# Performance work log

Measured on AMD Instinct MI355X. Metric: run time of the kernel, lower is better.

The kernel has to match this reference:

```python
import jax, jax.numpy as jnp
import numpy as np

B, S, D, H = 8, 1025, 768, 12
HD = D // H  # 64

def setup_inputs() -> dict:
    key = jax.random.key(0)
    ks = jax.random.split(key, 5)
    scale = 0.02
    return {
        "hidden_states": jax.random.normal(ks[0], (B, S, D), jnp.float32),
        "rel_bias": jax.random.normal(ks[1], (1, H, S, S), jnp.float32),
        "Wq": jax.random.normal(ks[2], (D, D), jnp.float32) * scale,
        "bq": jnp.zeros((D,), jnp.float32),
        "Wk": jax.random.normal(ks[3], (D, D), jnp.float32) * scale,
        "bk": jnp.zeros((D,), jnp.float32),
        "Wv": jax.random.normal(ks[4], (D, D), jnp.float32) * scale,
        "bv": jnp.zeros((D,), jnp.float32),
    }

def reference(hidden_states, rel_bias, Wq, bq, Wk, bk, Wv, bv):
    b, s, d = hidden_states.shape
    def split_heads(t):  # [B,S,D] -> [B,H,S,hd]
        return t.reshape(b, s, H, HD).transpose(0, 2, 1, 3)
    q = split_heads(hidden_states @ Wq + bq)
    k = split_heads(hidden_states @ Wk + bk)
    v = split_heads(hidden_states @ Wv + bv)
    inv_sqrt_hd = 1.0 / jnp.sqrt(jnp.asarray(HD, q.dtype))
    scores = jnp.einsum("bhqd,bhkd->bhqk", q, k) * inv_sqrt_hd
    scores = scores + rel_bias  # broadcast [1,H,S,S]
    probs = jax.nn.softmax(scores, axis=-1)
    ctx = jnp.einsum("bhqk,bhkd->bhqd", probs, v)
    out = ctx.transpose(0, 2, 1, 3).reshape(b, s, d)
    return out
```

## Files before the change

kernel.cpp:

```cpp
#include <hip/hip_runtime.h>

using f32x4  = __attribute__((ext_vector_type(4))) float;
using bf16x8 = __attribute__((ext_vector_type(8))) short;

#define SEQ 1025
#define NH  12

__device__ __forceinline__ unsigned short f2bf(float f) {
  unsigned u = __float_as_uint(f);
  u += 0x7FFFu + ((u >> 16) & 1u);
  return (unsigned short)(u >> 16);
}

__device__ __forceinline__ unsigned short f2bf_p(float f) {
  return (unsigned short)((__float_as_uint(f) + 0x8000u) >> 16);
}

__device__ __forceinline__ void async16(const void* g, void* s) {
  __builtin_amdgcn_global_load_lds(
      (const __attribute__((address_space(1))) void*)g,
      (__attribute__((address_space(3))) void*)s, 16, 0, 0);
}

__global__ __launch_bounds__(256) void conv_x(const float* __restrict__ X,
                                              ushort* __restrict__ Xb) {
  int t = blockIdx.x * 256 + threadIdx.x;
  if (t >= 8320 * 96) return;
  int row = t / 96;
  size_t e = (size_t)t * 8;
  union { uint4 q; ushort us[8]; } o;
  if (row < 8200) {
    float4 f0 = *(const float4*)(X + e);
    float4 f1 = *(const float4*)(X + e + 4);
    o.us[0] = f2bf(f0.x); o.us[1] = f2bf(f0.y); o.us[2] = f2bf(f0.z); o.us[3] = f2bf(f0.w);
    o.us[4] = f2bf(f1.x); o.us[5] = f2bf(f1.y); o.us[6] = f2bf(f1.z); o.us[7] = f2bf(f1.w);
  } else {
    o.q = make_uint4(0, 0, 0, 0);
  }
  *(uint4*)(Xb + e) = o.q;
}

__global__ __launch_bounds__(256) void pack_w(const float* __restrict__ Wq,
                                              const float* __restrict__ Wk,
                                              const float* __restrict__ Wv,
                                              ushort* __restrict__ Wt) {
  __shared__ float tile[32][33];
  const int nt = blockIdx.x;
  const int kt = blockIdx.y;
  const int sel = nt / 24;
  const int o0 = (nt - sel * 24) * 32;
  const int k0 = kt * 32;
  const float* W = sel == 0 ? Wq : sel == 1 ? Wk : Wv;
  const int t = threadIdx.x;
  const int x = t & 31, y = t >> 5;
  for (int p = 0; p < 4; ++p)
    tile[y + p * 8][x] = W[(size_t)(k0 + y + p * 8) * 768 + o0 + x];
  __syncthreads();
  for (int p = 0; p < 4; ++p) {
    const int nl = y + p * 8;
    Wt[(size_t)(nt * 32 + nl) * 768 + k0 + x] = f2bf(tile[x][nl]);
  }
}

__global__ __launch_bounds__(256) void pack_bias(const float* __restrict__ bq,
                                                 const float* __restrict__ bk,
                                                 const float* __restrict__ bv,
                                                 float* __restrict__ bc) {
  int t = blockIdx.x * 256 + threadIdx.x;
  if (t < 768) bc[t] = bq[t];
  else if (t < 1536) bc[t] = bk[t - 768];
  else if (t < 2304) bc[t] = bv[t - 1536];
}

__global__ __launch_bounds__(256, 2) void repack_bias_frag(
    const float* __restrict__ rel, float* __restrict__ bf) {
  __shared__ float lds[16][1092];
  const int h = blockIdx.x / 72;
  const int w = blockIdx.x - h * 72;
  const int t = threadIdx.x;
  const float* src = rel + (size_t)h * SEQ * SEQ;
  for (int r = 0; r < 16; ++r) {
    int q = w * 16 + r; if (q > 1024) q = 1024;
    const float* row = src + (size_t)q * SEQ;
    for (int c = t; c < 1088; c += 256)
      lds[r][c] = (c <= 1024) ? row[c] * 1.44269504f : -3.0e30f;
  }
  __syncthreads();
  float* dst = bf + ((size_t)h * 17 * 72 + w) * 1024;
  for (int kt = 0; kt < 17; ++kt) {
    float* d = dst + (size_t)kt * (72 * 1024);
    for (int j = t; j < 1024; j += 256) {
      int lane = j >> 4, e = j & 15;
      int ct = e >> 2, r2 = e & 3;
      int row = ((lane >> 4) << 2) + r2;
      int col = kt * 64 + ct * 16 + (lane & 15);
      d[j] = lds[row][col];
    }
  }
}

__global__ __launch_bounds__(256) void gemm_qkv(const ushort* __restrict__ A,
                                                const ushort* __restrict__ Bt,
                                                const float* __restrict__ bias,
                                                ushort* __restrict__ Qo,
                                                ushort* __restrict__ Ko,
                                                ushort* __restrict__ Vo) {
  __shared__ ushort a_sm[128 * 32];
  __shared__ ushort b_sm[128 * 32];
  const int t = threadIdx.x;
  const int lane = t & 63, wave = t >> 6;
  const int quad = lane >> 4, l16 = lane & 15;
  const int wrow = wave >> 1, wcol = wave & 1;
  const int m0 = blockIdx.x * 128, n0 = blockIdx.y * 128;

  f32x4 acc[4][4] = {};

  const ushort* a_g = A + (size_t)m0 * 768;
  const ushort* b_g = Bt + (size_t)n0 * 768;

  for (int k0 = 0; k0 < 768; k0 += 32) {
    __syncthreads();
    for (int r = 0; r < 2; ++r) {
      int c = r * 256 + t;
      int row = c >> 2;
      int colb = (c & 3) * 16;
      async16((const char*)(a_g + (size_t)row * 768 + k0) + colb, (char*)a_sm + c * 16);
      async16((const char*)(b_g + (size_t)row * 768 + k0) + colb, (char*)b_sm + c * 16);
    }
    __syncthreads();
    bf16x8 af[4], bfr[4];
    for (int i = 0; i < 4; ++i) {
      af[i]  = *(const bf16x8*)(a_sm + (wrow * 64 + i * 16 + l16) * 32 + quad * 8);
      bfr[i] = *(const bf16x8*)(b_sm + (wcol * 64 + i * 16 + l16) * 32 + quad * 8);
    }
    for (int i = 0; i < 4; ++i)
      for (int j = 0; j < 4; ++j)
        acc[i][j] = __builtin_amdgcn_mfma_f32_16x16x32_bf16(af[i], bfr[j], acc[i][j], 0, 0, 0);
  }

  for (int j = 0; j < 4; ++j) {
    const int gn = n0 + wcol * 64 + j * 16 + l16;
    const int sel = gn / 768;
    const int o = gn - sel * 768;
    const int hh = o >> 6, hd = o & 63;
    const float bv = bias[gn];
    ushort* dst = sel == 0 ? Qo : sel == 1 ? Ko : Vo;
    for (int i = 0; i < 4; ++i) {
      const int gmb = m0 + wrow * 64 + i * 16 + quad * 4;
      for (int r = 0; r < 4; ++r) {
        const int gm = gmb + r;
        if (gm < 8200) {
          const int bb = gm / 1025;
          const int ss = gm - bb * 1025;
          dst[(((size_t)(bb * NH + hh) * SEQ + ss) << 6) + hd] = f2bf(acc[i][j][r] + bv);
        }
      }
    }
  }
}

__global__ __launch_bounds__(256, 4) void attn(const ushort* __restrict__ Qb,
                                               const ushort* __restrict__ Kb,
                                               const ushort* __restrict__ Vb,
                                               const float* __restrict__ biasF,
                                               float* __restrict__ out) {
  __shared__ char smem[36864];
  ushort* p_sm = (ushort*)smem;
  ushort* k_sm = (ushort*)(smem + 18432);
  ushort* v_sm = (ushort*)(smem + 27648);

  const int t = threadIdx.x;
  const int lane = t & 63, wave = t >> 6;
  const int quad = lane >> 4, l16 = lane & 15;

  const int id = blockIdx.x;
  const int x = id & 7, s = id >> 3;
  const int Gg = s / 9, qt = s - Gg * 9;
  const int G = Gg * 8 + x;
  const int b = G / 12, h = G - b * 12;
  const int q0 = qt * 128;

  const size_t bh = (size_t)(b * NH + h) * SEQ * 64;
  const ushort* Qp = Qb + bh;
  const ushort* Kp = Kb + bh;
  const ushort* Vp = Vb + bh;

  uint4 kpre0, kpre1, vpre0, vpre1;
  const int vkp2 = t & 31, vhb = (t >> 5) * 8;

  auto issue_kv = [&](int kb) {
    {
      int c = t, row = c >> 3, cb = (c & 7) * 8;
      int rk = kb + row; if (rk > 1024) rk = 1024;
      kpre0 = *(const uint4*)(Kp + (size_t)rk * 64 + cb);
    }
    {
      int c = t + 256, row = c >> 3, cb = (c & 7) * 8;
      int rk = kb + row; if (rk > 1024) rk = 1024;
      kpre1 = *(const uint4*)(Kp + (size_t)rk * 64 + cb);
    }
    {
      int r0 = kb + vkp2 * 2;
      int r0c = r0 > 1024 ? 1024 : r0;
      int r1c = r0 + 1 > 1024 ? 1024 : r0 + 1;
      vpre0 = *(const uint4*)(Vp + (size_t)r0c * 64 + vhb);
      vpre1 = *(const uint4*)(Vp + (size_t)r1c * 64 + vhb);
    }
  };

  issue_kv(0);

  ushort* pw = p_sm + wave * (32 * 72);
  const int qbase = q0 + wave * 32;
  for (int i = 0; i < 4; ++i) {
    int c = lane + 64 * i;
    int row = c >> 3, cb = (c & 7) * 8;
    int rq = qbase + row; if (rq > 1024) rq = 1024;
    *(uint4*)(pw + row * 72 + cb) = *(const uint4*)(Qp + (size_t)rq * 64 + cb);
  }
  bf16x8 qf[2][2];
  for (int rt = 0; rt < 2; ++rt)
    for (int ks = 0; ks < 2; ++ks)
      qf[rt][ks] = *(const bf16x8*)(pw + (rt * 16 + l16) * 72 + ks * 32 + quad * 8);

  float lst[8] = {0, 0, 0, 0, 0, 0, 0, 0};
  f32x4 oacc[2][4] = {};
  const float c_scale = 0.18033688f;
  const float* bf_base = biasF +
      ((size_t)h * 17 * 72 + (qt * 8 + wave * 2)) * 1024 + (lane << 4);

  for (int kt = 0; kt < 17; ++kt) {
    __syncthreads();
    {
      int c = t;
      *(uint4*)(k_sm + (c >> 3) * 72 + (c & 7) * 8) = kpre0;
      c = t + 256;
      *(uint4*)(k_sm + (c >> 3) * 72 + (c & 7) * 8) = kpre1;
    }
    {
      union { uint4 q; ushort us[8]; } e0, e1;
      e0.q = vpre0; e1.q = vpre1;
      for (int e = 0; e < 8; ++e)
        *(unsigned*)(v_sm + (vhb + e) * 72 + vkp2 * 2) =
            (unsigned)e0.us[e] | ((unsigned)e1.us[e] << 16);
    }
    __syncthreads();

    const float* bfp = bf_base + (size_t)kt * (72 * 1024);
    f32x4 br[2][4];
    for (int rt = 0; rt < 2; ++rt)
      for (int ct = 0; ct < 4; ++ct)
        br[rt][ct] = *(const f32x4*)(bfp + rt * 1024 + ct * 4);

    if (kt < 16) issue_kv(kt * 64 + 64);

    f32x4 sc[2][4] = {};
    for (int ct = 0; ct < 4; ++ct)
      for (int ks = 0; ks < 2; ++ks) {
        bf16x8 kf = *(const bf16x8*)(k_sm + (ct * 16 + l16) * 72 + ks * 32 + quad * 8);
        sc[0][ct] = __builtin_amdgcn_mfma_f32_16x16x32_bf16(qf[0][ks], kf, sc[0][ct], 0, 0, 0);
        sc[1][ct] = __builtin_amdgcn_mfma_f32_16x16x32_bf16(qf[1][ks], kf, sc[1][ct], 0, 0, 0);
      }

    for (int rt = 0; rt < 2; ++rt)
      for (int ct = 0; ct < 4; ++ct)
        for (int r2 = 0; r2 < 4; ++r2) {
          float p = __builtin_amdgcn_exp2f(
              fmaf(sc[rt][ct][r2], c_scale, br[rt][ct][r2]));
          lst[rt * 4 + r2] += p;
          pw[(rt * 16 + quad * 4 + r2) * 72 + ct * 16 + l16] = f2bf_p(p);
        }

    for (int ks = 0; ks < 2; ++ks) {
      bf16x8 pf0 = *(const bf16x8*)(pw + l16 * 72 + ks * 32 + quad * 8);
      bf16x8 pf1 = *(const bf16x8*)(pw + (16 + l16) * 72 + ks * 32 + quad * 8);
      for (int c4 = 0; c4 < 4; ++c4) {
        bf16x8 vf = *(const bf16x8*)(v_sm + (c4 * 16 + l16) * 72 + ks * 32 + quad * 8);
        oacc[0][c4] = __builtin_amdgcn_mfma_f32_16x16x32_bf16(pf0, vf, oacc[0][c4], 0, 0, 0);
        oacc[1][c4] = __builtin_amdgcn_mfma_f32_16x16x32_bf16(pf1, vf, oacc[1][c4], 0, 0, 0);
      }
    }
  }

  for (int si = 0; si < 8; ++si) {
    float s2 = lst[si];
    s2 += __shfl_xor(s2, 1);
    s2 += __shfl_xor(s2, 2);
    s2 += __shfl_xor(s2, 4);
    s2 += __shfl_xor(s2, 8);
    lst[si] = s2;
  }
  for (int rt = 0; rt < 2; ++rt)
    for (int r2 = 0; r2 < 4; ++r2) {
      int sr = qbase + rt * 16 + quad * 4 + r2;
      if (sr < SEQ) {
        float inv = 1.0f / lst[rt * 4 + r2];
        float* op = out + ((size_t)b * SEQ + sr) * 768 + h * 64;
        for (int c4 = 0; c4 < 4; ++c4)
          op[c4 * 16 + l16] = oacc[rt][c4][r2] * inv;
      }
    }
}

extern "C" void kernel_launch(void* const* d_in, const int* in_sizes, int n_in,
                              void* d_out, int out_size, void* d_ws, size_t ws_size,
                              hipStream_t stream) {
  const float* X  = (const float*)d_in[0];
  const float* rb = (const float*)d_in[1];
  const float* Wq = (const float*)d_in[2];
  const float* bq = (const float*)d_in[3];
  const float* Wk = (const float*)d_in[4];
  const float* bk = (const float*)d_in[5];
  const float* Wv = (const float*)d_in[6];
  const float* bv = (const float*)d_in[7];
  float* out = (float*)d_out;
  char* ws = (char*)d_ws;

  ushort* Qb    = (ushort*)ws;
  ushort* Kb    = (ushort*)(ws + 12595200);
  ushort* Vb    = (ushort*)(ws + 25190400);
  ushort* Xb    = (ushort*)(ws + 37785600);
  ushort* Wt    = (ushort*)(ws + 50565120);
  float*  biasc = (float*)(ws + 54104064);
  float*  biasF = (float*)(ws + 37785600);

  conv_x<<<3120, 256, 0, stream>>>(X, Xb);
  pack_w<<<dim3(72, 24), 256, 0, stream>>>(Wq, Wk, Wv, Wt);
  pack_bias<<<9, 256, 0, stream>>>(bq, bk, bv, biasc);
  gemm_qkv<<<dim3(65, 18), 256, 0, stream>>>(Xb, Wt, biasc, Qb, Kb, Vb);
  repack_bias_frag<<<NH * 72, 256, 0, stream>>>(rb, biasF);
  attn<<<864, 256, 0, stream>>>(Qb, Kb, Vb, biasF, out);
}
```

Measured before the change: 369.6 us.

## Stage QKV epilogue through LDS, split bias repack, fuse bias pack

The QKV GEMM epilogue now stages bf16 results in shared memory and writes 16-byte vectorized rows per head, replacing scattered 2-byte stores. The relative-bias repack kernel is split into two column halves with a smaller LDS footprint, allowing more blocks per CU, and it writes f32x4 vectors. The bias-concatenation kernel is folded into pack_w to remove one launch. The cost is extra LDS and barriers in the GEMM epilogue.

Result: faster. 317.8 us (-14.0%).

```diff
diff --git a/kernel.cpp b/kernel.cpp
--- a/kernel.cpp
+++ b/kernel.cpp
@@ -43,7 +43,17 @@
 __global__ __launch_bounds__(256) void pack_w(const float* __restrict__ Wq,
                                               const float* __restrict__ Wk,
                                               const float* __restrict__ Wv,
-                                              ushort* __restrict__ Wt) {
+                                              ushort* __restrict__ Wt,
+                                              const float* __restrict__ bq,
+                                              const float* __restrict__ bk,
+                                              const float* __restrict__ bv,
+                                              float* __restrict__ bc) {
+  if (blockIdx.y == 0 && blockIdx.x < 9) {
+    int t2 = blockIdx.x * 256 + threadIdx.x;
+    if (t2 < 768) bc[t2] = bq[t2];
+    else if (t2 < 1536) bc[t2] = bk[t2 - 768];
+    else if (t2 < 2304) bc[t2] = bv[t2 - 1536];
+  }
   __shared__ float tile[32][33];
   const int nt = blockIdx.x;
   const int kt = blockIdx.y;
@@ -62,40 +72,38 @@
   }
 }
 
-__global__ __launch_bounds__(256) void pack_bias(const float* __restrict__ bq,
-                                                 const float* __restrict__ bk,
-                                                 const float* __restrict__ bv,
-                                                 float* __restrict__ bc) {
-  int t = blockIdx.x * 256 + threadIdx.x;
-  if (t < 768) bc[t] = bq[t];
-  else if (t < 1536) bc[t] = bk[t - 768];
-  else if (t < 2304) bc[t] = bv[t - 1536];
-}
-
-__global__ __launch_bounds__(256, 2) void repack_bias_frag(
+__global__ __launch_bounds__(256, 4) void repack_bias_frag(
     const float* __restrict__ rel, float* __restrict__ bf) {
-  __shared__ float lds[16][1092];
-  const int h = blockIdx.x / 72;
-  const int w = blockIdx.x - h * 72;
+  __shared__ float lds[16][580];
+  const int id = blockIdx.x;
+  const int half = id & 1;
+  const int hw = id >> 1;
+  const int h = hw / 72, w = hw - h * 72;
   const int t = threadIdx.x;
+  const int W = half ? 512 : 576;
+  const int cbase = half * 576;
   const float* src = rel + (size_t)h * SEQ * SEQ;
   for (int r = 0; r < 16; ++r) {
     int q = w * 16 + r; if (q > 1024) q = 1024;
     const float* row = src + (size_t)q * SEQ;
-    for (int c = t; c < 1088; c += 256)
-      lds[r][c] = (c <= 1024) ? row[c] * 1.44269504f : -3.0e30f;
+    for (int c = t; c < W; c += 256) {
+      int col = cbase + c;
+      lds[r][c] = (col <= 1024) ? row[col] * 1.44269504f : -3.0e30f;
+    }
   }
   __syncthreads();
-  float* dst = bf + ((size_t)h * 17 * 72 + w) * 1024;
-  for (int kt = 0; kt < 17; ++kt) {
-    float* d = dst + (size_t)kt * (72 * 1024);
-    for (int j = t; j < 1024; j += 256) {
-      int lane = j >> 4, e = j & 15;
-      int ct = e >> 2, r2 = e & 3;
-      int row = ((lane >> 4) << 2) + r2;
-      int col = kt * 64 + ct * 16 + (lane & 15);
-      d[j] = lds[row][col];
-    }
+  const int lane = t >> 2, ct = t & 3;
+  const int l16 = lane & 15, quad = lane >> 4;
+  const int nkt = half ? 8 : 9;
+  for (int ktl = 0; ktl < nkt; ++ktl) {
+    const int kt = half * 9 + ktl;
+    const int col = ktl * 64 + ct * 16 + l16;
+    f32x4 v;
+    v[0] = lds[quad * 4 + 0][col];
+    v[1] = lds[quad * 4 + 1][col];
+    v[2] = lds[quad * 4 + 2][col];
+    v[3] = lds[quad * 4 + 3][col];
+    *(f32x4*)(bf + (((size_t)h * 17 + kt) * 72 + w) * 1024 + lane * 16 + ct * 4) = v;
   }
 }
 
@@ -107,6 +115,7 @@
                                                 ushort* __restrict__ Vo) {
   __shared__ ushort a_sm[128 * 32];
   __shared__ ushort b_sm[128 * 32];
+  __shared__ ushort c_sm[64 * 136];
   const int t = threadIdx.x;
   const int lane = t & 63, wave = t >> 6;
   const int quad = lane >> 4, l16 = lane & 15;
@@ -138,22 +147,33 @@
         acc[i][j] = __builtin_amdgcn_mfma_f32_16x16x32_bf16(af[i], bfr[j], acc[i][j], 0, 0, 0);
   }
 
-  for (int j = 0; j < 4; ++j) {
-    const int gn = n0 + wcol * 64 + j * 16 + l16;
-    const int sel = gn / 768;
-    const int o = gn - sel * 768;
-    const int hh = o >> 6, hd = o & 63;
-    const float bv = bias[gn];
-    ushort* dst = sel == 0 ? Qo : sel == 1 ? Ko : Vo;
-    for (int i = 0; i < 4; ++i) {
-      const int gmb = m0 + wrow * 64 + i * 16 + quad * 4;
-      for (int r = 0; r < 4; ++r) {
-        const int gm = gmb + r;
-        if (gm < 8200) {
-          const int bb = gm / 1025;
-          const int ss = gm - bb * 1025;
-          dst[(((size_t)(bb * NH + hh) * SEQ + ss) << 6) + hd] = f2bf(acc[i][j][r] + bv);
-        }
+  const int sel = n0 / 768;
+  const int o0 = n0 - sel * 768;
+  const int hh0 = o0 >> 6;
+  ushort* dst = sel == 0 ? Qo : sel == 1 ? Ko : Vo;
+  float bvj[4];
+  for (int j = 0; j < 4; ++j) bvj[j] = bias[n0 + wcol * 64 + j * 16 + l16];
+
+  for (int p = 0; p < 2; ++p) {
+    __syncthreads();
+    if (wrow == p) {
+      for (int i = 0; i < 4; ++i)
+        for (int j = 0; j < 4; ++j)
+          for (int r = 0; r < 4; ++r)
+            c_sm[(i * 16 + quad * 4 + r) * 136 + wcol * 64 + j * 16 + l16] =
+                f2bf(acc[i][j][r] + bvj[j]);
+    }
+    __syncthreads();
+    const int head = t >> 7;
+    const int ci = t & 127;
+    for (int k = 0; k < 4; ++k) {
+      int ch = ci + 128 * k;
+      int row = ch >> 3, off = (ch & 7) * 8;
+      int gm = m0 + p * 64 + row;
+      if (gm < 8200) {
+        int bb = gm / 1025, ss = gm - bb * 1025;
+        uint4 v = *(const uint4*)(c_sm + row * 136 + head * 64 + off);
+        *(uint4*)(dst + (((size_t)(bb * NH + hh0 + head) * SEQ + ss) << 6) + off) = v;
       }
     }
   }
@@ -325,9 +345,8 @@
   float*  biasF = (float*)(ws + 37785600);
 
   conv_x<<<3120, 256, 0, stream>>>(X, Xb);
-  pack_w<<<dim3(72, 24), 256, 0, stream>>>(Wq, Wk, Wv, Wt);
-  pack_bias<<<9, 256, 0, stream>>>(bq, bk, bv, biasc);
+  pack_w<<<dim3(72, 24), 256, 0, stream>>>(Wq, Wk, Wv, Wt, bq, bk, bv, biasc);
   gemm_qkv<<<dim3(65, 18), 256, 0, stream>>>(Xb, Wt, biasc, Qb, Kb, Vb);
-  repack_bias_frag<<<NH * 72, 256, 0, stream>>>(rb, biasF);
+  repack_bias_frag<<<NH * 72 * 2, 256, 0, stream>>>(rb, biasF);
   attn<<<864, 256, 0, stream>>>(Qb, Kb, Vb, biasF, out);
 }
```
